# Optimization experiments

Hardware: AMD Instinct MI355X
Metric: run time of the kernel (lower is better)

## Reference

```python
import jax, jax.numpy as jnp
import numpy as np

B, T, D = 32, 1024, 512

def _xavier(key, shape):
    fan_in, fan_out = shape[1], shape[0]
    bound = float(np.sqrt(6.0 / (fan_in + fan_out)))
    return jax.random.uniform(key, shape, jnp.float32, -bound, bound)

def setup_inputs() -> dict:
    key = jax.random.key(0)
    ks = jax.random.split(key, 10)
    lin_bound = float(1.0 / np.sqrt(D))
    def lin(kw, kb):
        W = jax.random.uniform(kw, (D, D), jnp.float32, -lin_bound, lin_bound)
        b = jax.random.uniform(kb, (D,), jnp.float32, -lin_bound, lin_bound)
        return W, b
    Wk_w, Wk_b = lin(ks[0], ks[1])
    Wv_w, Wv_b = lin(ks[2], ks[3])
    Wq_w, Wq_b = lin(ks[4], ks[5])
    Wo_w, Wo_b = lin(ks[6], ks[7])
    w = _xavier(ks[8], (T, T))
    x = jax.random.normal(ks[9], (B, T, D), jnp.float32)
    return {"x": x, "Wk_w": Wk_w, "Wk_b": Wk_b, "Wv_w": Wv_w, "Wv_b": Wv_b,
            "Wq_w": Wq_w, "Wq_b": Wq_b, "w": w, "Wo_w": Wo_w, "Wo_b": Wo_b}

def reference(x, Wk_w, Wk_b, Wv_w, Wv_b, Wq_w, Wq_b, w, Wo_w, Wo_b):
    # K, V, Q: [B, T, D]  (torch Linear: x @ W.T + b)
    K = jnp.einsum('btd,ed->bte', x, Wk_w) + Wk_b
    V = jnp.einsum('btd,ed->bte', x, Wv_w) + Wv_b
    # exp_w: [T, T], row-wise max-stabilized position bias
    exp_w = jnp.exp(w - jnp.max(w, axis=-1, keepdims=True))
    # Faithful to original: max over dim=0 (batch dim) of K
    exp_K = jnp.exp(K - jnp.max(K, axis=0, keepdims=True))  # [B, T, D]
    num = jnp.einsum('ts,bsd->btd', exp_w, exp_K * V)
    den = jnp.einsum('ts,bsd->btd', exp_w, exp_K)
    Yt = num / den
    Q = jnp.einsum('btd,ed->bte', x, Wq_w) + Wq_b
    Yt = jax.nn.sigmoid(Q) * Yt
    out = jnp.einsum('btd,ed->bte', Yt, Wo_w) + Wo_b
    return out
```

## Files before the change

kernel.cpp:

```cpp
#include <hip/hip_runtime.h>
#include <stdint.h>

typedef unsigned short u16;
typedef __attribute__((ext_vector_type(4))) float f32x4;
typedef __attribute__((ext_vector_type(8))) __bf16 bf16x8;

__device__ __forceinline__ float b2f(u16 u) {
  union { unsigned int i; float f; } v; v.i = ((unsigned int)u) << 16; return v.f;
}
__device__ __forceinline__ u16 f2b(float f) {
  union { float f; unsigned int i; } v; v.f = f;
  unsigned int x = v.i;
  return (u16)((x + 0x7fffu + ((x >> 16) & 1u)) >> 16);
}

__device__ __forceinline__ void async_ld16(const u16* g, u16* l) {
  __builtin_amdgcn_global_load_lds((const __attribute__((address_space(1))) void*)g,
                                   (__attribute__((address_space(3))) void*)l, 16, 0, 0);
}

__global__ void detect_kernel(const u16* __restrict__ x, int* __restrict__ flag)
{
  const int tid = threadIdx.x;
  int found = 0;
  for (int i = tid; i < 32768; i += 256) {
    u16 u = x[i];
    if ((u & 0x7F80u) == 0x7F80u) found = 1;
  }
  unsigned long long m = __ballot(found != 0);
  __shared__ int sf[4];
  if ((tid & 63) == 0) sf[tid >> 6] = (m != 0ULL) ? 1 : 0;
  __syncthreads();
  if (tid == 0) flag[0] = (sf[0] | sf[1] | sf[2] | sf[3]);
}

__global__ __launch_bounds__(256)
void conv_kernel(const void* __restrict__ in, u16* __restrict__ out, long n,
                 const int* __restrict__ flag)
{
  const long i = ((long)blockIdx.x * 256 + threadIdx.x) * 8;
  if (i >= n) return;
  if (flag[0]) {
    const float* p = (const float*)in + i;
    u16 o[8];
#pragma unroll
    for (int j = 0; j < 8; j++) o[j] = f2b(p[j]);
    *(uint4*)(out + i) = *(const uint4*)o;
  } else {
    *(uint4*)(out + i) = *(const uint4*)((const u16*)in + i);
  }
}

#define BM 128
#define BN 128
#define BK 32

template<int EPI>
__global__ __launch_bounds__(256)
void gemm_bt(const u16* __restrict__ A, const u16* __restrict__ B,
             const void* __restrict__ bias, void* __restrict__ Cv,
             const int* __restrict__ flag,
             int M, int N, int K, long strideC)
{
  __shared__ __align__(16) u16 sA[BM * BK];
  __shared__ __align__(16) u16 sB[BN * BK];

  const int tid  = threadIdx.x;
  const int lane = tid & 63;
  const int wv   = tid >> 6;
  const int fl = flag[0];
  u16* Cb16 = (u16*)Cv;

  int bx = blockIdx.x, by = blockIdx.y;
  {
    const int nx = gridDim.x, ny = gridDim.y;
    if ((nx & 7) == 0) {
      const int d   = bx + nx * by;
      const int xcd = d & 7;
      const int s   = d >> 3;
      const int q   = s / ny;
      bx = xcd * (nx >> 3) + q;
      by = s - q * ny;
    }
  }
  const int m0 = bx * BM;
  const int n0 = by * BN;

  const int ldRow = wv * 32;
  const int lr = lane >> 2;
  const int lc = lane & 3;
  const int scol = (lc ^ ((lr >> 1) & 3)) * 8;
  const u16* gA = A + (long)(m0 + ldRow + lr) * K + scol;
  const u16* gB = B + (long)(n0 + ldRow + lr) * K + scol;
  u16* lA0 = sA + (ldRow + lr) * BK + lc * 8;
  u16* lA1 = sA + (ldRow + 16 + lr) * BK + lc * 8;
  u16* lB0 = sB + (ldRow + lr) * BK + lc * 8;
  u16* lB1 = sB + (ldRow + 16 + lr) * BK + lc * 8;

  f32x4 acc[4][4];
#pragma unroll
  for (int i = 0; i < 4; i++)
#pragma unroll
    for (int j = 0; j < 4; j++) acc[i][j] = (f32x4)0.0f;

  const int waveM = (wv >> 1) * 64;
  const int waveN = (wv & 1) * 64;
  const int quad  = lane >> 4;
  const int ll    = lane & 15;
  const int rs    = (quad ^ ((ll >> 1) & 3)) * 8;

  for (int k0 = 0; k0 < K; k0 += BK) {
    async_ld16(gA,          lA0);
    async_ld16(gA + 16 * K, lA1);
    async_ld16(gB,          lB0);
    async_ld16(gB + 16 * K, lB1);
    gA += BK; gB += BK;
    __syncthreads();

    bf16x8 aF[4], bF[4];
#pragma unroll
    for (int i = 0; i < 4; i++) {
      aF[i] = *(const bf16x8*)(sA + (waveM + i * 16 + ll) * BK + rs);
      bF[i] = *(const bf16x8*)(sB + (waveN + i * 16 + ll) * BK + rs);
    }
#pragma unroll
    for (int i = 0; i < 4; i++)
#pragma unroll
      for (int j = 0; j < 4; j++)
        acc[i][j] = __builtin_amdgcn_mfma_f32_16x16x32_bf16(aF[i], bF[j], acc[i][j], 0, 0, 0);
    __syncthreads();
  }

#pragma unroll
  for (int i = 0; i < 4; i++) {
    const int rowb = m0 + waveM + i * 16 + quad * 4;
#pragma unroll
    for (int j = 0; j < 4; j++) {
      const int col = n0 + waveN + j * 16 + ll;
      const float bv = fl ? ((const float*)bias)[col] : b2f(((const u16*)bias)[col]);
#pragma unroll
      for (int r = 0; r < 4; r++) {
        const long idx = (long)(rowb + r) * N + col;
        const float v = acc[i][j][r] + bv;
        if (EPI == 0) {
          Cb16[idx] = f2b(v);
        } else {
          const long g = strideC + idx;
          if (fl) ((float*)Cv)[g] = v;
          else    ((u16*)Cv)[g]   = f2b(v);
        }
      }
    }
  }
}

__global__ __launch_bounds__(256)
void gemm_proj3(const u16* __restrict__ A, const u16* __restrict__ Bw,
                const void* __restrict__ kb, const void* __restrict__ vb,
                const void* __restrict__ qb,
                u16* __restrict__ Kp, u16* __restrict__ Vp, u16* __restrict__ Qp,
                const int* __restrict__ flag, int M)
{
  const int KD = 512;
  __shared__ __align__(16) u16 sA[BM * BK];
  __shared__ __align__(16) u16 sB[BN * BK];

  const int tid  = threadIdx.x;
  const int lane = tid & 63;
  const int wv   = tid >> 6;
  const int fl = flag[0];

  int bx = blockIdx.x, by = blockIdx.y;
  {
    const int nx = gridDim.x, ny = gridDim.y;
    if ((nx & 7) == 0) {
      const int d   = bx + nx * by;
      const int xcd = d & 7;
      const int s   = d >> 3;
      const int q   = s / ny;
      bx = xcd * (nx >> 3) + q;
      by = s - q * ny;
    }
  }
  const int m0 = bx * BM;
  const int n0 = by * BN;

  const int ldRow = wv * 32;
  const int lr = lane >> 2;
  const int lc = lane & 3;
  const int scol = (lc ^ ((lr >> 1) & 3)) * 8;
  const u16* gA = A  + (long)(m0 + ldRow + lr) * KD + scol;
  const u16* gB = Bw + (long)(n0 + ldRow + lr) * KD + scol;
  u16* lA0 = sA + (ldRow + lr) * BK + lc * 8;
  u16* lA1 = sA + (ldRow + 16 + lr) * BK + lc * 8;
  u16* lB0 = sB + (ldRow + lr) * BK + lc * 8;
  u16* lB1 = sB + (ldRow + 16 + lr) * BK + lc * 8;

  f32x4 acc[4][4];
#pragma unroll
  for (int i = 0; i < 4; i++)
#pragma unroll
    for (int j = 0; j < 4; j++) acc[i][j] = (f32x4)0.0f;

  const int waveM = (wv >> 1) * 64;
  const int waveN = (wv & 1) * 64;
  const int quad  = lane >> 4;
  const int ll    = lane & 15;
  const int rs    = (quad ^ ((ll >> 1) & 3)) * 8;

  for (int k0 = 0; k0 < KD; k0 += BK) {
    async_ld16(gA,           lA0);
    async_ld16(gA + 16 * KD, lA1);
    async_ld16(gB,           lB0);
    async_ld16(gB + 16 * KD, lB1);
    gA += BK; gB += BK;
    __syncthreads();

    bf16x8 aF[4], bF[4];
#pragma unroll
    for (int i = 0; i < 4; i++) {
      aF[i] = *(const bf16x8*)(sA + (waveM + i * 16 + ll) * BK + rs);
      bF[i] = *(const bf16x8*)(sB + (waveN + i * 16 + ll) * BK + rs);
    }
#pragma unroll
    for (int i = 0; i < 4; i++)
#pragma unroll
      for (int j = 0; j < 4; j++)
        acc[i][j] = __builtin_amdgcn_mfma_f32_16x16x32_bf16(aF[i], bF[j], acc[i][j], 0, 0, 0);
    __syncthreads();
  }

#pragma unroll
  for (int i = 0; i < 4; i++) {
    const int rowb = m0 + waveM + i * 16 + quad * 4;
#pragma unroll
    for (int j = 0; j < 4; j++) {
      const int col = n0 + waveN + j * 16 + ll;
      const int sel = col >> 9;
      const int cs  = col & 511;
      const void* bp = (sel == 0) ? kb : (sel == 1) ? vb : qb;
      u16* dst = (sel == 0) ? Kp : (sel == 1) ? Vp : Qp;
      const float bv = fl ? ((const float*)bp)[cs] : b2f(((const u16*)bp)[cs]);
#pragma unroll
      for (int r = 0; r < 4; r++)
        dst[(long)(rowb + r) * 512 + cs] = f2b(acc[i][j][r] + bv);
    }
  }
}

#define AM 128
#define AN 64
#define ABK 32

__global__ __launch_bounds__(256, 2)
void gemm_aft(const u16* __restrict__ ew, const u16* __restrict__ Pt,
              const u16* __restrict__ PVt, const u16* __restrict__ Q,
              u16* __restrict__ Yt)
{
  const int T = 1024, D = 512;
  __shared__ __align__(16) u16 sA[AM * ABK];
  __shared__ __align__(16) u16 sB[AN * ABK];
  __shared__ __align__(16) u16 sC[AN * ABK];

  const int tid  = threadIdx.x;
  const int lane = tid & 63;
  const int wv   = tid >> 6;

  int xt = blockIdx.x, yt = blockIdx.y, zt = blockIdx.z;
  {
    const int nz = gridDim.z;
    const int d   = xt + (yt << 3) + (zt << 6);
    const int xcd = d & 7;
    const int s   = d >> 3;
    const int panel = xcd * nz + (s >> 3);
    xt = s & 7;
    yt = panel & 7;
    zt = panel >> 3;
  }
  const int b = zt;

  const u16* Ptb  = Pt  + (long)b * D * T;
  const u16* PVtb = PVt + (long)b * D * T;
  const u16* Qb   = Q   + (long)b * T * D;
  u16*       Ytb  = Yt  + (long)b * T * D;

  const int m0 = xt * AM;
  const int n0 = yt * AN;

  const int ldRow = wv * 16;
  const int lr = lane >> 2;
  const int lc = lane & 3;
  const int scol = (lc ^ ((lr >> 1) & 3)) * 8;
  const u16* gA = ew   + (long)(m0 + ldRow + lr) * T + scol;
  const u16* gB = Ptb  + (long)(n0 + ldRow + lr) * T + scol;
  const u16* gC = PVtb + (long)(n0 + ldRow + lr) * T + scol;
  u16* lA0 = sA + (ldRow + lr) * ABK + lc * 8;
  u16* lA1 = sA + (64 + ldRow + lr) * ABK + lc * 8;
  u16* lB0 = sB + (ldRow + lr) * ABK + lc * 8;
  u16* lC0 = sC + (ldRow + lr) * ABK + lc * 8;

  f32x4 accN[4][2], accD[4][2];
#pragma unroll
  for (int i = 0; i < 4; i++)
#pragma unroll
    for (int j = 0; j < 2; j++) { accN[i][j] = (f32x4)0.0f; accD[i][j] = (f32x4)0.0f; }

  const int waveM = (wv >> 1) * 64;
  const int waveN = (wv & 1) * 32;
  const int quad  = lane >> 4;
  const int ll    = lane & 15;
  const int rs    = (quad ^ ((ll >> 1) & 3)) * 8;

  for (int k0 = 0; k0 < T; k0 += ABK) {
    async_ld16(gA,          lA0);
    async_ld16(gA + 64 * T, lA1);
    async_ld16(gB,          lB0);
    async_ld16(gC,          lC0);
    gA += ABK; gB += ABK; gC += ABK;
    __syncthreads();

    bf16x8 aF[4], bF[2], cF[2];
#pragma unroll
    for (int i = 0; i < 4; i++)
      aF[i] = *(const bf16x8*)(sA + (waveM + i * 16 + ll) * ABK + rs);
#pragma unroll
    for (int j = 0; j < 2; j++) {
      bF[j] = *(const bf16x8*)(sB + (waveN + j * 16 + ll) * ABK + rs);
      cF[j] = *(const bf16x8*)(sC + (waveN + j * 16 + ll) * ABK + rs);
    }
#pragma unroll
    for (int i = 0; i < 4; i++)
#pragma unroll
      for (int j = 0; j < 2; j++) {
        accD[i][j] = __builtin_amdgcn_mfma_f32_16x16x32_bf16(aF[i], bF[j], accD[i][j], 0, 0, 0);
        accN[i][j] = __builtin_amdgcn_mfma_f32_16x16x32_bf16(aF[i], cF[j], accN[i][j], 0, 0, 0);
      }
    __syncthreads();
  }

#pragma unroll
  for (int i = 0; i < 4; i++) {
    const int rowb = m0 + waveM + i * 16 + quad * 4;
#pragma unroll
    for (int j = 0; j < 2; j++) {
      const int col = n0 + waveN + j * 16 + ll;
#pragma unroll
      for (int r = 0; r < 4; r++) {
        const long idx = (long)(rowb + r) * D + col;
        const float q  = b2f(Qb[idx]);
        const float t  = __expf(-q);
        const float rc = __builtin_amdgcn_rcpf(accD[i][j][r] * (1.0f + t));
        Ytb[idx] = f2b(accN[i][j][r] * rc);
      }
    }
  }
}

__global__ __launch_bounds__(256)
void expw_kernel(const void* __restrict__ w, u16* __restrict__ ew,
                 const int* __restrict__ flag)
{
  const int fl = flag[0];
  const int t = blockIdx.x;
  const int tid = threadIdx.x;
  float v[4];
  float m = -1e30f;
#pragma unroll
  for (int i = 0; i < 4; i++) {
    const long idx = (long)t * 1024 + tid + i * 256;
    float val = fl ? ((const float*)w)[idx] : b2f(((const u16*)w)[idx]);
    v[i] = val; m = fmaxf(m, val);
  }
#pragma unroll
  for (int off = 32; off > 0; off >>= 1) m = fmaxf(m, __shfl_xor(m, off, 64));
  __shared__ float sm[4];
  if ((tid & 63) == 0) sm[tid >> 6] = m;
  __syncthreads();
  m = fmaxf(fmaxf(sm[0], sm[1]), fmaxf(sm[2], sm[3]));
  u16* orow = ew + (long)t * 1024;
#pragma unroll
  for (int i = 0; i < 4; i++) orow[tid + i * 256] = f2b(__expf(v[i] - m));
}

__global__ __launch_bounds__(256)
void kmax_kernel(const u16* __restrict__ K, u16* __restrict__ Km)
{
  const long TD = 1024L * 512;
  const long base = ((long)blockIdx.x * 256 + threadIdx.x) * 8;
  float m[8];
#pragma unroll
  for (int j = 0; j < 8; j++) m[j] = -1e30f;
  for (int b = 0; b < 32; b++) {
    uint4 u = *(const uint4*)(K + b * TD + base);
    const u16* p = (const u16*)&u;
#pragma unroll
    for (int j = 0; j < 8; j++) m[j] = fmaxf(m[j], b2f(p[j]));
  }
  u16 outv[8];
#pragma unroll
  for (int j = 0; j < 8; j++) outv[j] = f2b(m[j]);
  *(uint4*)(Km + base) = *(const uint4*)outv;
}

__global__ __launch_bounds__(256)
void pexp_kernel(const u16* __restrict__ K, const u16* __restrict__ V,
                 const u16* __restrict__ Km,
                 u16* __restrict__ Pt, u16* __restrict__ PVt)
{
  const int T = 1024, D = 512;
  const long TD = (long)T * D;
  const int s0 = blockIdx.x * 64;
  const int d0 = blockIdx.y * 64;
  const int b  = blockIdx.z;
  __shared__ u16 lp[64 * 66];
  __shared__ u16 lpv[64 * 66];
  const int tid  = threadIdx.x;
  const int srow = tid >> 3;
  const int c8   = (tid & 7) * 8;

#pragma unroll
  for (int h = 0; h < 2; h++) {
    const int s = srow + h * 32;
    const long gidx = (long)b * TD + (long)(s0 + s) * D + d0 + c8;
    uint4 ku = *(const uint4*)(K + gidx);
    uint4 vu = *(const uint4*)(V + gidx);
    uint4 mu = *(const uint4*)(Km + (long)(s0 + s) * D + d0 + c8);
    const u16* kp = (const u16*)&ku;
    const u16* vp = (const u16*)&vu;
    const u16* mp = (const u16*)&mu;
#pragma unroll
    for (int j = 0; j < 8; j++) {
      float p  = __expf(b2f(kp[j]) - b2f(mp[j]));
      float pv = p * b2f(vp[j]);
      lp[s * 66 + c8 + j]  = f2b(p);
      lpv[s * 66 + c8 + j] = f2b(pv);
    }
  }
  __syncthreads();

  const int lane = tid & 63;
  const int wv   = tid >> 6;
#pragma unroll
  for (int it = 0; it < 16; it++) {
    const int d = wv * 16 + it;
    const long oidx = (long)b * TD + (long)(d0 + d) * T + s0 + lane;
    Pt[oidx]  = lp[lane * 66 + d];
    PVt[oidx] = lpv[lane * 66 + d];
  }
}

extern "C" void kernel_launch(void* const* d_in, const int* in_sizes, int n_in,
                              void* d_out, int out_size, void* d_ws, size_t ws_size,
                              hipStream_t stream)
{
  const int B = 32, T = 1024, D = 512;
  const long TD = (long)T * D;
  const void* x    = d_in[0];
  const void* Wk_w = d_in[1];
  const void* Wk_b = d_in[2];
  const void* Wv_w = d_in[3];
  const void* Wv_b = d_in[4];
  const void* Wq_w = d_in[5];
  const void* Wq_b = d_in[6];
  const void* w    = d_in[7];
  const void* Wo_w = d_in[8];
  const void* Wo_b = d_in[9];

  char* ws = (char*)d_ws;
  const size_t MB = 1024 * 1024;
  u16* xb    = (u16*)(ws + 0);
  u16* Kbuf  = (u16*)(ws + 32 * MB);
  u16* ewb   = (u16*)(ws + 64 * MB);
  u16* kmb   = (u16*)(ws + 66 * MB);
  u16* Wpack = (u16*)(ws + 67 * MB);
  u16* Wvb   = Wpack + 512 * 512;
  u16* Wqb   = Wpack + 2 * 512 * 512;
  u16* Wob   = (u16*)(ws + 68 * MB + 512 * 1024);
  int* flag  = (int*)(ws + 69 * MB);
  u16* Ytb   = Kbuf;

  dim3 blk(256);

  detect_kernel<<<dim3(1), blk, 0, stream>>>((const u16*)x, flag);
  conv_kernel<<<dim3(8192), blk, 0, stream>>>(x,    xb,    (long)B * T * D, flag);
  conv_kernel<<<dim3(128),  blk, 0, stream>>>(Wk_w, Wpack, (long)D * D, flag);
  conv_kernel<<<dim3(128),  blk, 0, stream>>>(Wv_w, Wvb,   (long)D * D, flag);
  conv_kernel<<<dim3(128),  blk, 0, stream>>>(Wq_w, Wqb,   (long)D * D, flag);
  conv_kernel<<<dim3(128),  blk, 0, stream>>>(Wo_w, Wob,   (long)D * D, flag);
  expw_kernel<<<dim3(1024), blk, 0, stream>>>(w, ewb, flag);

  if (ws_size >= 200 * MB) {
    u16* Vb   = (u16*)(ws + 70 * MB);
    u16* Qb   = (u16*)(ws + 102 * MB);
    u16* Ptb  = (u16*)(ws + 134 * MB);
    u16* PVtb = (u16*)(ws + 166 * MB);

    gemm_proj3<<<dim3((B * T) / 128, 12), blk, 0, stream>>>(
        xb, Wpack, Wk_b, Wv_b, Wq_b, Kbuf, Vb, Qb, flag, B * T);

    kmax_kernel<<<dim3(256), blk, 0, stream>>>(Kbuf, kmb);
    pexp_kernel<<<dim3(16, 8, 32), blk, 0, stream>>>(Kbuf, Vb, kmb, Ptb, PVtb);

    gemm_aft<<<dim3(T / AM, D / AN, 32), blk, 0, stream>>>(ewb, Ptb, PVtb, Qb, Ytb);

    gemm_bt<3><<<dim3((B * T) / 128, D / 128), blk, 0, stream>>>(
        Ytb, Wob, Wo_b, d_out, flag, B * T, D, D, 0);
  } else {
    const int NB = 4, NC = B / NB;
    char* ck = ws + 70 * MB;
    const size_t cb = (size_t)NB * TD * sizeof(u16);
    u16* Vc   = (u16*)(ck);
    u16* Ptc  = (u16*)(ck + cb);
    u16* PVtc = (u16*)(ck + 2 * cb);
    u16* Qc   = (u16*)(ck + 3 * cb);
    u16* Ytc  = Vc;

    gemm_bt<0><<<dim3((B * T) / 128, D / 128), blk, 0, stream>>>(
        xb, Wpack, Wk_b, Kbuf, flag, B * T, D, D, 0);
    kmax_kernel<<<dim3(256), blk, 0, stream>>>(Kbuf, kmb);

    dim3 gP((NB * T) / 128, D / 128, 1);
    dim3 gA(T / AM, D / AN, NB);
    for (int c = 0; c < NC; c++) {
      const long off = (long)c * NB * TD;
      gemm_bt<0><<<gP, blk, 0, stream>>>(xb + off, Wvb, Wv_b, Vc, flag, NB * T, D, D, 0);
      gemm_bt<0><<<gP, blk, 0, stream>>>(xb + off, Wqb, Wq_b, Qc, flag, NB * T, D, D, 0);
      pexp_kernel<<<dim3(16, 8, NB), blk, 0, stream>>>(Kbuf + off, Vc, kmb, Ptc, PVtc);
      gemm_aft<<<gA, blk, 0, stream>>>(ewb, Ptc, PVtc, Qc, Ytc);
      gemm_bt<3><<<gP, blk, 0, stream>>>(Ytc, Wob, Wo_b, d_out, flag, NB * T, D, D, off);
    }
  }
}
```

Measured before the change: 383.5 us.

## Double-buffer LDS tiles in GEMM kernels and merge weight conversion launches

Converts the three MFMA GEMM kernels (gemm_bt, gemm_proj3, gemm_aft) to double-buffered shared memory. The next K-tile's async global-to-LDS load is issued before computing on the current tile, which removes one barrier per iteration and overlaps load latency with MFMA work. It also fuses the four weight conversion launches into a single conv4_kernel to cut launch overhead. The trade-off is twice the LDS footprint per block, which may lower occupancy.

```diff
diff --git a/kernel.cpp b/kernel.cpp
--- a/kernel.cpp
+++ b/kernel.cpp
@@ -51,6 +51,29 @@
   }
 }
 
+__global__ __launch_bounds__(256)
+void conv4_kernel(const void* __restrict__ i0, const void* __restrict__ i1,
+                  const void* __restrict__ i2, const void* __restrict__ i3,
+                  u16* __restrict__ o0, u16* __restrict__ o1,
+                  u16* __restrict__ o2, u16* __restrict__ o3,
+                  const int* __restrict__ flag)
+{
+  const int sel = blockIdx.x >> 7;
+  const int blk = blockIdx.x & 127;
+  const void* in = (sel == 0) ? i0 : (sel == 1) ? i1 : (sel == 2) ? i2 : i3;
+  u16* out = (sel == 0) ? o0 : (sel == 1) ? o1 : (sel == 2) ? o2 : o3;
+  const long i = ((long)blk * 256 + threadIdx.x) * 8;
+  if (flag[0]) {
+    const float* p = (const float*)in + i;
+    u16 o[8];
+#pragma unroll
+    for (int j = 0; j < 8; j++) o[j] = f2b(p[j]);
+    *(uint4*)(out + i) = *(const uint4*)o;
+  } else {
+    *(uint4*)(out + i) = *(const uint4*)((const u16*)in + i);
+  }
+}
+
 #define BM 128
 #define BN 128
 #define BK 32
@@ -62,8 +85,8 @@
              const int* __restrict__ flag,
              int M, int N, int K, long strideC)
 {
-  __shared__ __align__(16) u16 sA[BM * BK];
-  __shared__ __align__(16) u16 sB[BN * BK];
+  __shared__ __align__(16) u16 sA[2][BM * BK];
+  __shared__ __align__(16) u16 sB[2][BN * BK];
 
   const int tid  = threadIdx.x;
   const int lane = tid & 63;
@@ -92,10 +115,8 @@
   const int scol = (lc ^ ((lr >> 1) & 3)) * 8;
   const u16* gA = A + (long)(m0 + ldRow + lr) * K + scol;
   const u16* gB = B + (long)(n0 + ldRow + lr) * K + scol;
-  u16* lA0 = sA + (ldRow + lr) * BK + lc * 8;
-  u16* lA1 = sA + (ldRow + 16 + lr) * BK + lc * 8;
-  u16* lB0 = sB + (ldRow + lr) * BK + lc * 8;
-  u16* lB1 = sB + (ldRow + 16 + lr) * BK + lc * 8;
+  const int off0 = (ldRow + lr) * BK + lc * 8;
+  const int off1 = (ldRow + 16 + lr) * BK + lc * 8;
 
   f32x4 acc[4][4];
 #pragma unroll
@@ -109,26 +130,38 @@
   const int ll    = lane & 15;
   const int rs    = (quad ^ ((ll >> 1) & 3)) * 8;
 
-  for (int k0 = 0; k0 < K; k0 += BK) {
-    async_ld16(gA,          lA0);
-    async_ld16(gA + 16 * K, lA1);
-    async_ld16(gB,          lB0);
-    async_ld16(gB + 16 * K, lB1);
-    gA += BK; gB += BK;
+  async_ld16(gA,          sA[0] + off0);
+  async_ld16(gA + 16 * K, sA[0] + off1);
+  async_ld16(gB,          sB[0] + off0);
+  async_ld16(gB + 16 * K, sB[0] + off1);
+  gA += BK; gB += BK;
+
+  const int NT = K / BK;
+  for (int t = 0; t < NT; ++t) {
     __syncthreads();
-
+    const int cur = t & 1;
+    if (t + 1 < NT) {
+      u16* dA = sA[cur ^ 1];
+      u16* dB = sB[cur ^ 1];
+      async_ld16(gA,          dA + off0);
+      async_ld16(gA + 16 * K, dA + off1);
+      async_ld16(gB,          dB + off0);
+      async_ld16(gB + 16 * K, dB + off1);
+      gA += BK; gB += BK;
+    }
+    const u16* rA = sA[cur];
+    const u16* rB = sB[cur];
     bf16x8 aF[4], bF[4];
 #pragma unroll
     for (int i = 0; i < 4; i++) {
-      aF[i] = *(const bf16x8*)(sA + (waveM + i * 16 + ll) * BK + rs);
-      bF[i] = *(const bf16x8*)(sB + (waveN + i * 16 + ll) * BK + rs);
+      aF[i] = *(const bf16x8*)(rA + (waveM + i * 16 + ll) * BK + rs);
+      bF[i] = *(const bf16x8*)(rB + (waveN + i * 16 + ll) * BK + rs);
     }
 #pragma unroll
     for (int i = 0; i < 4; i++)
 #pragma unroll
       for (int j = 0; j < 4; j++)
         acc[i][j] = __builtin_amdgcn_mfma_f32_16x16x32_bf16(aF[i], bF[j], acc[i][j], 0, 0, 0);
-    __syncthreads();
   }
 
 #pragma unroll
@@ -162,8 +195,8 @@
                 const int* __restrict__ flag, int M)
 {
   const int KD = 512;
-  __shared__ __align__(16) u16 sA[BM * BK];
-  __shared__ __align__(16) u16 sB[BN * BK];
+  __shared__ __align__(16) u16 sA[2][BM * BK];
+  __shared__ __align__(16) u16 sB[2][BN * BK];
 
   const int tid  = threadIdx.x;
   const int lane = tid & 63;
@@ -191,10 +224,8 @@
   const int scol = (lc ^ ((lr >> 1) & 3)) * 8;
   const u16* gA = A  + (long)(m0 + ldRow + lr) * KD + scol;
   const u16* gB = Bw + (long)(n0 + ldRow + lr) * KD + scol;
-  u16* lA0 = sA + (ldRow + lr) * BK + lc * 8;
-  u16* lA1 = sA + (ldRow + 16 + lr) * BK + lc * 8;
-  u16* lB0 = sB + (ldRow + lr) * BK + lc * 8;
-  u16* lB1 = sB + (ldRow + 16 + lr) * BK + lc * 8;
+  const int off0 = (ldRow + lr) * BK + lc * 8;
+  const int off1 = (ldRow + 16 + lr) * BK + lc * 8;
 
   f32x4 acc[4][4];
 #pragma unroll
@@ -208,26 +239,38 @@
   const int ll    = lane & 15;
   const int rs    = (quad ^ ((ll >> 1) & 3)) * 8;
 
-  for (int k0 = 0; k0 < KD; k0 += BK) {
-    async_ld16(gA,           lA0);
-    async_ld16(gA + 16 * KD, lA1);
-    async_ld16(gB,           lB0);
-    async_ld16(gB + 16 * KD, lB1);
-    gA += BK; gB += BK;
+  async_ld16(gA,           sA[0] + off0);
+  async_ld16(gA + 16 * KD, sA[0] + off1);
+  async_ld16(gB,           sB[0] + off0);
+  async_ld16(gB + 16 * KD, sB[0] + off1);
+  gA += BK; gB += BK;
+
+  const int NT = KD / BK;
+  for (int t = 0; t < NT; ++t) {
     __syncthreads();
-
+    const int cur = t & 1;
+    if (t + 1 < NT) {
+      u16* dA = sA[cur ^ 1];
+      u16* dB = sB[cur ^ 1];
+      async_ld16(gA,           dA + off0);
+      async_ld16(gA + 16 * KD, dA + off1);
+      async_ld16(gB,           dB + off0);
+      async_ld16(gB + 16 * KD, dB + off1);
+      gA += BK; gB += BK;
+    }
+    const u16* rA = sA[cur];
+    const u16* rB = sB[cur];
     bf16x8 aF[4], bF[4];
 #pragma unroll
     for (int i = 0; i < 4; i++) {
-      aF[i] = *(const bf16x8*)(sA + (waveM + i * 16 + ll) * BK + rs);
-      bF[i] = *(const bf16x8*)(sB + (waveN + i * 16 + ll) * BK + rs);
+      aF[i] = *(const bf16x8*)(rA + (waveM + i * 16 + ll) * BK + rs);
+      bF[i] = *(const bf16x8*)(rB + (waveN + i * 16 + ll) * BK + rs);
     }
 #pragma unroll
     for (int i = 0; i < 4; i++)
 #pragma unroll
       for (int j = 0; j < 4; j++)
         acc[i][j] = __builtin_amdgcn_mfma_f32_16x16x32_bf16(aF[i], bF[j], acc[i][j], 0, 0, 0);
-    __syncthreads();
   }
 
 #pragma unroll
@@ -258,9 +301,9 @@
               u16* __restrict__ Yt)
 {
   const int T = 1024, D = 512;
-  __shared__ __align__(16) u16 sA[AM * ABK];
-  __shared__ __align__(16) u16 sB[AN * ABK];
-  __shared__ __align__(16) u16 sC[AN * ABK];
+  __shared__ __align__(16) u16 sA[2][AM * ABK];
+  __shared__ __align__(16) u16 sB[2][AN * ABK];
+  __shared__ __align__(16) u16 sC[2][AN * ABK];
 
   const int tid  = threadIdx.x;
   const int lane = tid & 63;
@@ -294,10 +337,9 @@
   const u16* gA = ew   + (long)(m0 + ldRow + lr) * T + scol;
   const u16* gB = Ptb  + (long)(n0 + ldRow + lr) * T + scol;
   const u16* gC = PVtb + (long)(n0 + ldRow + lr) * T + scol;
-  u16* lA0 = sA + (ldRow + lr) * ABK + lc * 8;
-  u16* lA1 = sA + (64 + ldRow + lr) * ABK + lc * 8;
-  u16* lB0 = sB + (ldRow + lr) * ABK + lc * 8;
-  u16* lC0 = sC + (ldRow + lr) * ABK + lc * 8;
+  const int offA0 = (ldRow + lr) * ABK + lc * 8;
+  const int offA1 = (64 + ldRow + lr) * ABK + lc * 8;
+  const int offB0 = (ldRow + lr) * ABK + lc * 8;
 
   f32x4 accN[4][2], accD[4][2];
 #pragma unroll
@@ -311,22 +353,37 @@
   const int ll    = lane & 15;
   const int rs    = (quad ^ ((ll >> 1) & 3)) * 8;
 
-  for (int k0 = 0; k0 < T; k0 += ABK) {
-    async_ld16(gA,          lA0);
-    async_ld16(gA + 64 * T, lA1);
-    async_ld16(gB,          lB0);
-    async_ld16(gC,          lC0);
-    gA += ABK; gB += ABK; gC += ABK;
+  async_ld16(gA,          sA[0] + offA0);
+  async_ld16(gA + 64 * T, sA[0] + offA1);
+  async_ld16(gB,          sB[0] + offB0);
+  async_ld16(gC,          sC[0] + offB0);
+  gA += ABK; gB += ABK; gC += ABK;
+
+  const int NT = T / ABK;
+  for (int t = 0; t < NT; ++t) {
     __syncthreads();
-
+    const int cur = t & 1;
+    if (t + 1 < NT) {
+      u16* dA = sA[cur ^ 1];
+      u16* dB = sB[cur ^ 1];
+      u16* dC = sC[cur ^ 1];
+      async_ld16(gA,          dA + offA0);
+      async_ld16(gA + 64 * T, dA + offA1);
+      async_ld16(gB,          dB + offB0);
+      async_ld16(gC,          dC + offB0);
+      gA += ABK; gB += ABK; gC += ABK;
+    }
+    const u16* rA = sA[cur];
+    const u16* rB = sB[cur];
+    const u16* rC = sC[cur];
     bf16x8 aF[4], bF[2], cF[2];
 #pragma unroll
     for (int i = 0; i < 4; i++)
-      aF[i] = *(const bf16x8*)(sA + (waveM + i * 16 + ll) * ABK + rs);
+      aF[i] = *(const bf16x8*)(rA + (waveM + i * 16 + ll) * ABK + rs);
 #pragma unroll
     for (int j = 0; j < 2; j++) {
-      bF[j] = *(const bf16x8*)(sB + (waveN + j * 16 + ll) * ABK + rs);
-      cF[j] = *(const bf16x8*)(sC + (waveN + j * 16 + ll) * ABK + rs);
+      bF[j] = *(const bf16x8*)(rB + (waveN + j * 16 + ll) * ABK + rs);
+      cF[j] = *(const bf16x8*)(rC + (waveN + j * 16 + ll) * ABK + rs);
     }
 #pragma unroll
     for (int i = 0; i < 4; i++)
@@ -335,7 +392,6 @@
         accD[i][j] = __builtin_amdgcn_mfma_f32_16x16x32_bf16(aF[i], bF[j], accD[i][j], 0, 0, 0);
         accN[i][j] = __builtin_amdgcn_mfma_f32_16x16x32_bf16(aF[i], cF[j], accN[i][j], 0, 0, 0);
       }
-    __syncthreads();
   }
 
 #pragma unroll
@@ -482,11 +538,9 @@
   dim3 blk(256);
 
   detect_kernel<<<dim3(1), blk, 0, stream>>>((const u16*)x, flag);
-  conv_kernel<<<dim3(8192), blk, 0, stream>>>(x,    xb,    (long)B * T * D, flag);
-  conv_kernel<<<dim3(128),  blk, 0, stream>>>(Wk_w, Wpack, (long)D * D, flag);
-  conv_kernel<<<dim3(128),  blk, 0, stream>>>(Wv_w, Wvb,   (long)D * D, flag);
-  conv_kernel<<<dim3(128),  blk, 0, stream>>>(Wq_w, Wqb,   (long)D * D, flag);
-  conv_kernel<<<dim3(128),  blk, 0, stream>>>(Wo_w, Wob,   (long)D * D, flag);
+  conv_kernel<<<dim3(8192), blk, 0, stream>>>(x, xb, (long)B * T * D, flag);
+  conv4_kernel<<<dim3(512), blk, 0, stream>>>(Wk_w, Wv_w, Wq_w, Wo_w,
+                                              Wpack, Wvb, Wqb, Wob, flag);
   expw_kernel<<<dim3(1024), blk, 0, stream>>>(w, ewb, flag);
 
   if (ws_size >= 200 * MB) {
```

Result: no change. 379.6 us (-1.0%).
